# Kernel optimization log

Measured on AMD Instinct MI355X. Metric: run time of the kernel, lower is better.

## Reference

```python
import jax, jax.numpy as jnp
import numpy as np

BN_EPS = 1e-3


def _knn_group(p1, p2, k):
    # p1, p2: [N, 3]. For each point in p1 find k nearest in p2.
    d2 = (jnp.sum(p1 * p1, -1)[:, None] + jnp.sum(p2 * p2, -1)[None, :]
          - 2.0 * (p1 @ p2.T))                      # [N, N]
    _, idx = jax.lax.top_k(-d2, k)                   # [N, k]
    nn = p2[idx]                                     # [N, k, 3]
    resi = nn - p1[:, None, :]                       # [N, k, 3]
    dist = jnp.linalg.norm(resi, axis=-1, keepdims=True)
    feat = jnp.concatenate([resi, dist], axis=-1)    # [N, k, 4]
    return feat, nn


def _conv_bn_relu(x, W, b, g, be):
    # x: [B, Cin, N, K]; 1x1 conv == channel matmul, BN uses batch stats (train mode)
    y = jnp.einsum('oi,binK->bonK', W, x) + b[None, :, None, None]
    m = jnp.mean(y, axis=(0, 2, 3), keepdims=True)
    v = jnp.var(y, axis=(0, 2, 3), keepdims=True)
    y = g[None, :, None, None] * (y - m) * jax.lax.rsqrt(v + BN_EPS) + be[None, :, None, None]
    return jax.nn.relu(y)


def setup_inputs() -> dict:
    key = jax.random.key(0)
    ks = jax.random.split(key, 8)
    B, N, k = 4, 4096, 32
    C = [4, 64, 64, 128]
    inp = {
        'points1': jax.random.normal(ks[0], (B, 3, N), jnp.float32),
        'points2': jax.random.normal(ks[1], (B, 3, N), jnp.float32),
        'k': k,
        't': jax.random.uniform(ks[2], (B,), jnp.float32),
    }
    for i in range(3):
        kw = jax.random.fold_in(ks[3], i)
        inp[f'W{i+1}'] = jax.random.normal(kw, (C[i + 1], C[i]), jnp.float32) * (1.0 / np.sqrt(C[i]))
        inp[f'b{i+1}'] = jnp.zeros((C[i + 1],), jnp.float32)
        inp[f'g{i+1}'] = jnp.ones((C[i + 1],), jnp.float32)
        inp[f'be{i+1}'] = jnp.zeros((C[i + 1],), jnp.float32)
    return inp


def reference(points1, points2, k, t, W1, b1, g1, be1, W2, b2, g2, be2, W3, b3, g3, be3):
    p1 = jnp.transpose(points1, (0, 2, 1))           # [B, N, 3]
    p2 = jnp.transpose(points2, (0, 2, 1))
    knn = jax.vmap(_knn_group, in_axes=(0, 0, None))
    f1, nn1 = knn(p1, p1, k)                          # [B, N, k, 4], [B, N, k, 3]
    f2, nn2 = knn(p1, p2, k)
    feats = jnp.concatenate([f1, f2], axis=2)         # [B, N, 2k, 4]
    grouped = jnp.concatenate([nn1, nn2], axis=2)     # [B, N, 2k, 3]
    x = jnp.transpose(feats, (0, 3, 1, 2))            # [B, 4, N, 2k]
    x = _conv_bn_relu(x, W1, b1, g1, be1)
    x = _conv_bn_relu(x, W2, b2, g2, be2)
    x = _conv_bn_relu(x, W3, b3, g3, be3)             # [B, 128, N, 2k]
    scores = jnp.max(x, axis=1)                       # [B, N, 2k]
    w = jax.nn.softmax(scores, axis=-1)               # [B, N, 2k]
    fused = jnp.einsum('bnk,bnkc->bcn', w, grouped)   # [B, 3, N]
    return fused
```

## Files before the change

### kernel.cpp

```cpp
#include <hip/hip_runtime.h>
#include <hip/hip_bf16.h>

#define B_   4
#define N_   4096
#define KNN_ 32
#define KK_  64
#define MTOT 1048576
#define BN_EPS 1e-3f

typedef unsigned int u32;
typedef unsigned long long u64;
typedef __attribute__((ext_vector_type(8))) short bf16x8;
typedef __attribute__((ext_vector_type(4))) float f32x4;

__device__ __forceinline__ ushort f2bf_bits(float f) {
    u32 b = __float_as_uint(f);
    b += 0x7fffu + ((b >> 16) & 1u);
    return (ushort)(b >> 16);
}

__global__ __launch_bounds__(256, 3) void knn_kernel(
    const float* __restrict__ p1, const float* __restrict__ p2,
    float* __restrict__ feats, float* __restrict__ mom)
{
    __shared__ float2 cxy[N_];
    __shared__ float  cz[N_];
    __shared__ float  part[4][14];

    const int tid  = threadIdx.x;
    const int wave = tid >> 6, lane = tid & 63;
    const int pb    = blockIdx.x / 96;
    const int chunk = blockIdx.x % 96;
    const int pr = pb >> 2, b = pb & 3;
    const int start = (chunk * 4096) / 96;
    const int end   = ((chunk + 1) * 4096) / 96;

    const float* srcb = (pr ? p2 : p1) + (size_t)b * 3 * N_;
    for (int n = tid; n < N_; n += 256) {
        float x = srcb[n], y = srcb[N_ + n], z = srcb[2*N_ + n];
        cxy[n] = make_float2(x, y);
        cz[n]  = z;
    }
    __syncthreads();

    const float* p1b = p1 + (size_t)b * 3 * N_;
    const u64 below = (1ull << lane) - 1ull;

    float mm[14];
    #pragma unroll
    for (int s = 0; s < 14; ++s) mm[s] = 0.f;

    for (int n = start + wave; n < end; n += 4) {
        float qx, qy, qz;
        if (pr == 0) { float2 q = cxy[n]; qx = q.x; qy = q.y; qz = cz[n]; }
        else         { qx = p1b[n]; qy = p1b[N_ + n]; qz = p1b[2*N_ + n]; }
        const float s1 = fmaf(qx, qx, fmaf(qy, qy, qz*qz));

        u32 keys[64];
        u32 a0 = 0xFFFFFFFFu, a1 = 0xFFFFFFFFu, a2 = 0xFFFFFFFFu, a3 = 0xFFFFFFFFu;
        u32 b0 = 0xFFFFFFFFu, b1 = 0xFFFFFFFFu, b2 = 0xFFFFFFFFu, b3 = 0xFFFFFFFFu;
        #pragma unroll
        for (int j = 0; j < 32; ++j) {
            {
                float2 cA = cxy[j * 64 + lane];
                float  zA = cz[j * 64 + lane];
                float cw  = fmaf(cA.x, cA.x, fmaf(cA.y, cA.y, zA*zA));
                float dot = fmaf(qx, cA.x, fmaf(qy, cA.y, qz * zA));
                float d2  = fmaf(-2.0f, dot, s1 + cw);
                u32 u = __float_as_uint(d2);
                u32 key = u ^ (u32)(((int)u >> 31) | 0x80000000);
                keys[j] = key;
                a3 = min(a3, key);
                u32 t;
                t = min(a2, a3); a3 = max(a2, a3); a2 = t;
                t = min(a1, a2); a2 = max(a1, a2); a1 = t;
                t = min(a0, a1); a1 = max(a0, a1); a0 = t;
            }
            {
                float2 cB = cxy[(j + 32) * 64 + lane];
                float  zB = cz[(j + 32) * 64 + lane];
                float cw  = fmaf(cB.x, cB.x, fmaf(cB.y, cB.y, zB*zB));
                float dot = fmaf(qx, cB.x, fmaf(qy, cB.y, qz * zB));
                float d2  = fmaf(-2.0f, dot, s1 + cw);
                u32 u = __float_as_uint(d2);
                u32 key = u ^ (u32)(((int)u >> 31) | 0x80000000);
                keys[j + 32] = key;
                b3 = min(b3, key);
                u32 t;
                t = min(b2, b3); b3 = max(b2, b3); b2 = t;
                t = min(b1, b2); b2 = max(b1, b2); b1 = t;
                t = min(b0, b1); b1 = max(b0, b1); b0 = t;
            }
        }
        u32 k0 = a0, k1 = a1, k2 = a2, k3 = a3;
        #pragma unroll
        for (int m = 0; m < 4; ++m) {
            u32 x = (m == 0) ? b0 : (m == 1) ? b1 : (m == 2) ? b2 : b3;
            k3 = min(k3, x);
            u32 t;
            t = min(k2, k3); k3 = max(k2, k3); k2 = t;
            t = min(k1, k2); k2 = max(k1, k2); k1 = t;
            t = min(k0, k1); k1 = max(k0, k1); k0 = t;
        }

        u32 mn = k0, mx = k3;
        #pragma unroll
        for (int off = 1; off < 64; off <<= 1) {
            mn = min(mn, (u32)__shfl_xor((int)mn, off, 64));
            mx = max(mx, (u32)__shfl_xor((int)mx, off, 64));
        }
        u32 lo = mn, hi = mx;
        while (lo < hi) {
            u32 mid = lo + ((hi - lo) >> 1);
            int c = __popcll(__ballot(k0 <= mid)) + __popcll(__ballot(k1 <= mid))
                  + __popcll(__ballot(k2 <= mid)) + __popcll(__ballot(k3 <= mid));
            if (c >= 32) hi = mid; else lo = mid + 1;
        }
        u32 T = lo;

        int nl;
        if (__ballot(k3 <= T) == 0ull) {
            nl = __popcll(__ballot(k0 < T)) + __popcll(__ballot(k1 < T))
               + __popcll(__ballot(k2 < T)) + __popcll(__ballot(k3 < T));
        } else {
            nl = 0;
            #pragma unroll
            for (int j = 0; j < 64; ++j) nl += __popcll(__ballot(keys[j] < T));
            if (nl > 31) {
                lo = 0u; hi = T;
                while (lo < hi) {
                    u32 mid = lo + ((hi - lo) >> 1);
                    int c = 0;
                    #pragma unroll
                    for (int j = 0; j < 64; ++j) c += __popcll(__ballot(keys[j] <= mid));
                    if (c >= 32) hi = mid; else lo = mid + 1;
                }
                T = lo;
                nl = 0;
                #pragma unroll
                for (int j = 0; j < 64; ++j) nl += __popcll(__ballot(keys[j] < T));
            }
        }
        const int need_eq = 32 - nl;

        float* fout = feats + ((size_t)(b * N_ + n) * KK_ + pr * KNN_) * 4;
        int base = 0, eq_seen = 0;
        #pragma unroll
        for (int j = 0; j < 64; ++j) {
            u32 key = keys[j];
            bool lt = key < T;
            bool eq = key == T;
            u64 mlt = __ballot(lt);
            u64 meq = __ballot(eq);
            if (mlt | meq) {
                int slot = -1;
                if (lt) slot = base + __popcll(mlt & below);
                else if (eq) {
                    int es = eq_seen + __popcll(meq & below);
                    if (es < need_eq) slot = nl + es;
                }
                if (slot >= 0) {
                    float2 cx2 = cxy[j * 64 + lane];
                    float  cz1 = cz[j * 64 + lane];
                    float rx = cx2.x - qx, ry = cx2.y - qy, rz = cz1 - qz;
                    float dist = sqrtf(fmaf(rx, rx, fmaf(ry, ry, rz*rz)));
                    *(float4*)(fout + slot * 4) = make_float4(rx, ry, rz, dist);
                    mm[0] += rx; mm[1] += ry; mm[2] += rz; mm[3] += dist;
                    mm[4]  = fmaf(rx, rx, mm[4]);   mm[5]  = fmaf(rx, ry, mm[5]);
                    mm[6]  = fmaf(rx, rz, mm[6]);   mm[7]  = fmaf(rx, dist, mm[7]);
                    mm[8]  = fmaf(ry, ry, mm[8]);   mm[9]  = fmaf(ry, rz, mm[9]);
                    mm[10] = fmaf(ry, dist, mm[10]); mm[11] = fmaf(rz, rz, mm[11]);
                    mm[12] = fmaf(rz, dist, mm[12]); mm[13] = fmaf(dist, dist, mm[13]);
                }
                base    += __popcll(mlt);
                eq_seen += __popcll(meq);
            }
        }
    }

    #pragma unroll
    for (int s = 0; s < 14; ++s) {
        #pragma unroll
        for (int off = 1; off < 64; off <<= 1) mm[s] += __shfl_xor(mm[s], off, 64);
    }
    if (lane == 0) {
        #pragma unroll
        for (int s = 0; s < 14; ++s) part[wave][s] = mm[s];
    }
    __syncthreads();
    if (tid < 14) {
        float v = part[0][tid] + part[1][tid] + part[2][tid] + part[3][tid];
        atomicAdd(&mom[tid * 16], v);
    }
}

__global__ __launch_bounds__(256) void conv2_mfma(
    const float* __restrict__ feats,
    const float* __restrict__ W1,
    const float* __restrict__ g1, const float* __restrict__ be1,
    const float* __restrict__ W2,
    const float* __restrict__ mom,
    ushort* __restrict__ y2F, float* __restrict__ s2S, float* __restrict__ s2Q)
{
    __shared__ float statS[64], statQ[64];
    const int tid = threadIdx.x;
    const int wid = tid >> 6, l = tid & 63, q = l >> 4, i = l & 15;
    if (tid < 64) { statS[tid] = 0.f; statQ[tid] = 0.f; }

    const float invM = 1.0f / MTOT;
    const float M0 = mom[0*16], M1 = mom[1*16], M2 = mom[2*16], M3 = mom[3*16];
    const float Sxx = mom[4*16],  Sxy = mom[5*16],  Sxz = mom[6*16],  Sxd = mom[7*16];
    const float Syy = mom[8*16],  Syz = mom[9*16],  Syd = mom[10*16];
    const float Szz = mom[11*16], Szd = mom[12*16], Sdd = mom[13*16];

    float4 w1f[16];
    float  c1v[16];
    #pragma unroll
    for (int h = 0; h < 2; ++h)
      #pragma unroll
      for (int j = 0; j < 8; ++j) {
        int ci = h*32 + q*8 + j;
        float w0 = W1[ci*4+0], w1 = W1[ci*4+1], w2 = W1[ci*4+2], w3 = W1[ci*4+3];
        float meanf = (w0*M0 + w1*M1 + w2*M2 + w3*M3) * invM;
        float qq = w0*(w0*Sxx + 2.f*(w1*Sxy + w2*Sxz + w3*Sxd))
                 + w1*(w1*Syy + 2.f*(w2*Syz + w3*Syd))
                 + w2*(w2*Szz + 2.f*w3*Szd)
                 + w3*w3*Sdd;
        float var = qq * invM - meanf * meanf;
        float sc  = g1[ci] * rsqrtf(var + BN_EPS);
        w1f[h*8+j] = make_float4(sc*w0, sc*w1, sc*w2, sc*w3);
        c1v[h*8+j] = fmaf(-sc, meanf, be1[ci]);
      }
    bf16x8 a2[4][2];
    #pragma unroll
    for (int t = 0; t < 4; ++t)
      #pragma unroll
      for (int h = 0; h < 2; ++h)
        #pragma unroll
        for (int j = 0; j < 8; ++j)
          a2[t][h][j] = (short)f2bf_bits(W2[(t*16 + i)*64 + h*32 + q*8 + j]);

    float ssum[16], ssq[16];
    #pragma unroll
    for (int s = 0; s < 16; ++s) { ssum[s] = 0.f; ssq[s] = 0.f; }
    __syncthreads();

    for (int r16 = 0; r16 < 16; ++r16) {
        const int row = blockIdx.x * 16 + r16;
        float4 f = ((const float4*)feats)[row*64 + wid*16 + i];
        bf16x8 xb[2];
        #pragma unroll
        for (int h = 0; h < 2; ++h)
          #pragma unroll
          for (int j = 0; j < 8; ++j) {
            float4 w = w1f[h*8+j];
            float x = fmaxf(fmaf(w.x, f.x, fmaf(w.y, f.y, fmaf(w.z, f.z, fmaf(w.w, f.w, c1v[h*8+j])))), 0.f);
            xb[h][j] = (short)f2bf_bits(x);
          }
        f32x4 acc[4];
        #pragma unroll
        for (int t = 0; t < 4; ++t) acc[t] = (f32x4){0.f,0.f,0.f,0.f};
        #pragma unroll
        for (int t = 0; t < 4; ++t) {
            acc[t] = __builtin_amdgcn_mfma_f32_16x16x32_bf16(a2[t][0], xb[0], acc[t], 0, 0, 0);
            acc[t] = __builtin_amdgcn_mfma_f32_16x16x32_bf16(a2[t][1], xb[1], acc[t], 0, 0, 0);
        }
        ushort* wp = y2F + row*4096 + wid*1024 + q*64 + i*4;
        #pragma unroll
        for (int t = 0; t < 4; ++t) {
            #pragma unroll
            for (int reg = 0; reg < 4; ++reg) {
                float y = acc[t][reg];
                ssum[t*4+reg] += y;
                ssq[t*4+reg]  = fmaf(y, y, ssq[t*4+reg]);
            }
            uint2 pk;
            pk.x = (u32)f2bf_bits(acc[t][0]) | ((u32)f2bf_bits(acc[t][1]) << 16);
            pk.y = (u32)f2bf_bits(acc[t][2]) | ((u32)f2bf_bits(acc[t][3]) << 16);
            *(uint2*)(wp + t*256) = pk;
        }
    }
    #pragma unroll
    for (int s = 0; s < 16; ++s) {
        #pragma unroll
        for (int off = 1; off < 16; off <<= 1) {
            ssum[s] += __shfl_xor(ssum[s], off, 64);
            ssq[s]  += __shfl_xor(ssq[s],  off, 64);
        }
    }
    if (i == 0) {
        #pragma unroll
        for (int s = 0; s < 16; ++s) {
            int co = (s >> 2)*16 + q*4 + (s & 3);
            atomicAdd(&statS[co], ssum[s]);
            atomicAdd(&statQ[co], ssq[s]);
        }
    }
    __syncthreads();
    if (tid < 64) { atomicAdd(&s2S[tid], statS[tid]); atomicAdd(&s2Q[tid], statQ[tid]); }
}

template<bool FINAL>
__global__ __launch_bounds__(256) void conv3_mfma(
    const ushort* __restrict__ y2F,
    const float* __restrict__ g2, const float* __restrict__ be2,
    const float* __restrict__ W3,
    const float* __restrict__ g3, const float* __restrict__ be3,
    const float* __restrict__ s2S, const float* __restrict__ s2Q,
    float* __restrict__ s3S, float* __restrict__ s3Q,
    const float4* __restrict__ feats4, const float* __restrict__ p1,
    float* __restrict__ outp)
{
    __shared__ float statS[128], statQ[128];
    __shared__ float sc3L[128], sh3L[128];
    __shared__ float scoreL[2][64];

    const int tid = threadIdx.x;
    const int wid = tid >> 6, l = tid & 63, q = l >> 4, i = l & 15;

    if (!FINAL) {
        if (tid < 128) { statS[tid] = 0.f; statQ[tid] = 0.f; }
    } else if (tid < 128) {
        float m  = s3S[tid] * (1.0f / MTOT);
        float v  = s3Q[tid] * (1.0f / MTOT) - m * m;
        float sc = g3[tid] * rsqrtf(v + BN_EPS);
        sc3L[tid] = sc;
        sh3L[tid] = fmaf(-sc, m, be3[tid]);
    }

    float sc2v[16], sh2v[16];
    #pragma unroll
    for (int h = 0; h < 2; ++h)
      #pragma unroll
      for (int j = 0; j < 8; ++j) {
        int ci = h*32 + q*8 + j;
        float m  = s2S[ci] * (1.0f / MTOT);
        float v  = s2Q[ci] * (1.0f / MTOT) - m * m;
        float sc = g2[ci] * rsqrtf(v + BN_EPS);
        sc2v[h*8+j] = sc;
        sh2v[h*8+j] = fmaf(-sc, m, be2[ci]);
      }
    bf16x8 a3[8][2];
    #pragma unroll
    for (int t = 0; t < 8; ++t)
      #pragma unroll
      for (int h = 0; h < 2; ++h)
        #pragma unroll
        for (int j = 0; j < 8; ++j)
          a3[t][h][j] = (short)f2bf_bits(W3[(t*16 + i)*64 + h*32 + q*8 + j]);

    float ssum[32], ssq[32];
    if (!FINAL) {
        #pragma unroll
        for (int s = 0; s < 32; ++s) { ssum[s] = 0.f; ssq[s] = 0.f; }
    }
    __syncthreads();

    for (int r16 = 0; r16 < 16; ++r16) {
        const int row = blockIdx.x * 16 + r16;
        const ushort* rp = y2F + row*4096 + wid*1024 + q*128 + i*4;
        uint2 u00 = *(const uint2*)(rp);
        uint2 u01 = *(const uint2*)(rp + 64);
        uint2 u10 = *(const uint2*)(rp + 512);
        uint2 u11 = *(const uint2*)(rp + 576);

        bf16x8 xb[2];
        #pragma unroll
        for (int h = 0; h < 2; ++h) {
            u32 w0 = (h == 0) ? u00.x : u10.x;
            u32 w1 = (h == 0) ? u00.y : u10.y;
            u32 w2 = (h == 0) ? u01.x : u11.x;
            u32 w3 = (h == 0) ? u01.y : u11.y;
            float xf[8];
            xf[0] = __uint_as_float(w0 << 16); xf[1] = __uint_as_float(w0 & 0xffff0000u);
            xf[2] = __uint_as_float(w1 << 16); xf[3] = __uint_as_float(w1 & 0xffff0000u);
            xf[4] = __uint_as_float(w2 << 16); xf[5] = __uint_as_float(w2 & 0xffff0000u);
            xf[6] = __uint_as_float(w3 << 16); xf[7] = __uint_as_float(w3 & 0xffff0000u);
            #pragma unroll
            for (int j = 0; j < 8; ++j) {
                float x = fmaxf(fmaf(sc2v[h*8+j], xf[j], sh2v[h*8+j]), 0.f);
                xb[h][j] = (short)f2bf_bits(x);
            }
        }
        f32x4 acc[8];
        #pragma unroll
        for (int t = 0; t < 8; ++t) acc[t] = (f32x4){0.f,0.f,0.f,0.f};
        #pragma unroll
        for (int t = 0; t < 8; ++t) {
            acc[t] = __builtin_amdgcn_mfma_f32_16x16x32_bf16(a3[t][0], xb[0], acc[t], 0, 0, 0);
            acc[t] = __builtin_amdgcn_mfma_f32_16x16x32_bf16(a3[t][1], xb[1], acc[t], 0, 0, 0);
        }

        if (!FINAL) {
            #pragma unroll
            for (int t = 0; t < 8; ++t)
              #pragma unroll
              for (int reg = 0; reg < 4; ++reg) {
                float y = acc[t][reg];
                ssum[t*4+reg] += y;
                ssq[t*4+reg]  = fmaf(y, y, ssq[t*4+reg]);
              }
        } else {
            float mx = -3.4e38f;
            #pragma unroll
            for (int t = 0; t < 8; ++t) {
                float4 s4 = *(const float4*)&sc3L[t*16 + q*4];
                float4 h4 = *(const float4*)&sh3L[t*16 + q*4];
                mx = fmaxf(mx, fmaf(s4.x, acc[t][0], h4.x));
                mx = fmaxf(mx, fmaf(s4.y, acc[t][1], h4.y));
                mx = fmaxf(mx, fmaf(s4.z, acc[t][2], h4.z));
                mx = fmaxf(mx, fmaf(s4.w, acc[t][3], h4.w));
            }
            mx = fmaxf(mx, __shfl_xor(mx, 16, 64));
            mx = fmaxf(mx, __shfl_xor(mx, 32, 64));
            mx = fmaxf(mx, 0.f);
            if (q == 0) scoreL[r16 & 1][wid*16 + i] = mx;
            __syncthreads();
            if (wid == 0) {
                float sc = scoreL[r16 & 1][l];
                float m2 = sc;
                #pragma unroll
                for (int off = 1; off < 64; off <<= 1) m2 = fmaxf(m2, __shfl_xor(m2, off, 64));
                float e = __expf(sc - m2);
                float se = e;
                #pragma unroll
                for (int off = 1; off < 64; off <<= 1) se += __shfl_xor(se, off, 64);
                float w = e / se;
                const int bb = row >> 12, n = row & 4095;
                float qx = p1[(size_t)bb*3*N_ + n];
                float qy = p1[(size_t)bb*3*N_ + N_ + n];
                float qz = p1[(size_t)bb*3*N_ + 2*N_ + n];
                float4 f4 = feats4[row*64 + l];
                float ox = w * (f4.x + qx), oy = w * (f4.y + qy), oz = w * (f4.z + qz);
                #pragma unroll
                for (int off = 1; off < 64; off <<= 1) {
                    ox += __shfl_xor(ox, off, 64);
                    oy += __shfl_xor(oy, off, 64);
                    oz += __shfl_xor(oz, off, 64);
                }
                if (l == 0) {
                    outp[bb*3*N_ + 0*N_ + n] = ox;
                    outp[bb*3*N_ + 1*N_ + n] = oy;
                    outp[bb*3*N_ + 2*N_ + n] = oz;
                }
            }
        }
    }

    if (!FINAL) {
        #pragma unroll
        for (int s = 0; s < 32; ++s) {
            #pragma unroll
            for (int off = 1; off < 16; off <<= 1) {
                ssum[s] += __shfl_xor(ssum[s], off, 64);
                ssq[s]  += __shfl_xor(ssq[s],  off, 64);
            }
        }
        if (i == 0) {
            #pragma unroll
            for (int s = 0; s < 32; ++s) {
                int co = (s >> 2)*16 + q*4 + (s & 3);
                atomicAdd(&statS[co], ssum[s]);
                atomicAdd(&statQ[co], ssq[s]);
            }
        }
        __syncthreads();
        if (tid < 128) { atomicAdd(&s3S[tid], statS[tid]); atomicAdd(&s3Q[tid], statQ[tid]); }
    }
}

extern "C" void kernel_launch(void* const* d_in, const int* in_sizes, int n_in,
                              void* d_out, int out_size, void* d_ws, size_t ws_size,
                              hipStream_t stream)
{
    const float* p1  = (const float*)d_in[0];
    const float* p2  = (const float*)d_in[1];
    const float* W1  = (const float*)d_in[4];
    const float* g1  = (const float*)d_in[6];
    const float* be1 = (const float*)d_in[7];
    const float* W2  = (const float*)d_in[8];
    const float* g2  = (const float*)d_in[10];
    const float* be2 = (const float*)d_in[11];
    const float* W3  = (const float*)d_in[12];
    const float* g3  = (const float*)d_in[14];
    const float* be3 = (const float*)d_in[15];

    char* ws = (char*)d_ws;
    const size_t OFF_FEATS = 4096;
    const size_t OFF_Y2    = OFF_FEATS + (size_t)MTOT * 4 * 4;
    const size_t NEEDED    = OFF_Y2 + (size_t)MTOT * 64 * 2;
    if (ws_size < NEEDED) return;

    float* s2S = (float*)(ws + 512);  float* s2Q = (float*)(ws + 768);
    float* s3S = (float*)(ws + 1024); float* s3Q = (float*)(ws + 1536);
    float* mom = (float*)(ws + 2048);
    float* feats = (float*)(ws + OFF_FEATS);
    ushort* y2F  = (ushort*)(ws + OFF_Y2);

    hipMemsetAsync(ws, 0, 4096, stream);

    knn_kernel<<<768, 256, 0, stream>>>(p1, p2, feats, mom);
    conv2_mfma<<<1024, 256, 0, stream>>>(feats, W1, g1, be1, W2, mom,
                                         y2F, s2S, s2Q);
    conv3_mfma<false><<<1024, 256, 0, stream>>>(y2F, g2, be2, W3, g3, be3,
                                                s2S, s2Q, s3S, s3Q,
                                                nullptr, nullptr, nullptr);
    conv3_mfma<true><<<1024, 256, 0, stream>>>(y2F, g2, be2, W3, g3, be3,
                                               s2S, s2Q, s3S, s3Q,
                                               (const float4*)feats, p1,
                                               (float*)d_out);
}
```

Baseline: 511.8 us.

## Write BN2-ReLU activations back in place and split conv3 output channels across waves

The conv3 stats pass now applies the BN2 scale/shift, ReLU and bf16 rounding, then writes the activated values back into the y2 buffer in place. The final pass can then feed those values straight into the MFMAs without redoing the normalization. Work is also repartitioned so each wave handles two point-tiles and half of the 128 output channels, which halves the A-fragment register footprint (a3 drops from 8x2 to 4x2). The cost is an extra 128 MB of bf16 global writes in the stats pass. There is also an in-place read-then-write hazard, guarded only by a block-level __syncthreads, that depends on the two wave halves reading identical addresses.

Result: faster. 477.4 us (-6.7%).

```diff
diff --git a/kernel.cpp b/kernel.cpp
--- a/kernel.cpp
+++ b/kernel.cpp
@@ -300,33 +300,18 @@
     if (tid < 64) { atomicAdd(&s2S[tid], statS[tid]); atomicAdd(&s2Q[tid], statQ[tid]); }
 }
 
-template<bool FINAL>
-__global__ __launch_bounds__(256) void conv3_mfma(
-    const ushort* __restrict__ y2F,
+__global__ __launch_bounds__(256) void conv3_stats(
+    ushort* __restrict__ y2F,
     const float* __restrict__ g2, const float* __restrict__ be2,
     const float* __restrict__ W3,
-    const float* __restrict__ g3, const float* __restrict__ be3,
     const float* __restrict__ s2S, const float* __restrict__ s2Q,
-    float* __restrict__ s3S, float* __restrict__ s3Q,
-    const float4* __restrict__ feats4, const float* __restrict__ p1,
-    float* __restrict__ outp)
+    float* __restrict__ s3S, float* __restrict__ s3Q)
 {
     __shared__ float statS[128], statQ[128];
-    __shared__ float sc3L[128], sh3L[128];
-    __shared__ float scoreL[2][64];
-
     const int tid = threadIdx.x;
-    const int wid = tid >> 6, l = tid & 63, q = l >> 4, i = l & 15;
-
-    if (!FINAL) {
-        if (tid < 128) { statS[tid] = 0.f; statQ[tid] = 0.f; }
-    } else if (tid < 128) {
-        float m  = s3S[tid] * (1.0f / MTOT);
-        float v  = s3Q[tid] * (1.0f / MTOT) - m * m;
-        float sc = g3[tid] * rsqrtf(v + BN_EPS);
-        sc3L[tid] = sc;
-        sh3L[tid] = fmaf(-sc, m, be3[tid]);
-    }
+    const int w = tid >> 6, l = tid & 63, q = l >> 4, i = l & 15;
+    const int ph = w >> 1, oh = w & 1;
+    if (tid < 128) { statS[tid] = 0.f; statQ[tid] = 0.f; }
 
     float sc2v[16], sh2v[16];
     #pragma unroll
@@ -340,132 +325,188 @@
         sc2v[h*8+j] = sc;
         sh2v[h*8+j] = fmaf(-sc, m, be2[ci]);
       }
-    bf16x8 a3[8][2];
-    #pragma unroll
-    for (int t = 0; t < 8; ++t)
+    bf16x8 a3[4][2];
+    #pragma unroll
+    for (int t = 0; t < 4; ++t)
       #pragma unroll
       for (int h = 0; h < 2; ++h)
         #pragma unroll
         for (int j = 0; j < 8; ++j)
-          a3[t][h][j] = (short)f2bf_bits(W3[(t*16 + i)*64 + h*32 + q*8 + j]);
-
-    float ssum[32], ssq[32];
-    if (!FINAL) {
-        #pragma unroll
-        for (int s = 0; s < 32; ++s) { ssum[s] = 0.f; ssq[s] = 0.f; }
-    }
-    __syncthreads();
+          a3[t][h][j] = (short)f2bf_bits(W3[((oh*4 + t)*16 + i)*64 + h*32 + q*8 + j]);
+
+    float ssum[16], ssq[16];
+    #pragma unroll
+    for (int s = 0; s < 16; ++s) { ssum[s] = 0.f; ssq[s] = 0.f; }
 
     for (int r16 = 0; r16 < 16; ++r16) {
         const int row = blockIdx.x * 16 + r16;
-        const ushort* rp = y2F + row*4096 + wid*1024 + q*128 + i*4;
-        uint2 u00 = *(const uint2*)(rp);
-        uint2 u01 = *(const uint2*)(rp + 64);
-        uint2 u10 = *(const uint2*)(rp + 512);
-        uint2 u11 = *(const uint2*)(rp + 576);
-
-        bf16x8 xb[2];
-        #pragma unroll
-        for (int h = 0; h < 2; ++h) {
-            u32 w0 = (h == 0) ? u00.x : u10.x;
-            u32 w1 = (h == 0) ? u00.y : u10.y;
-            u32 w2 = (h == 0) ? u01.x : u11.x;
-            u32 w3 = (h == 0) ? u01.y : u11.y;
-            float xf[8];
-            xf[0] = __uint_as_float(w0 << 16); xf[1] = __uint_as_float(w0 & 0xffff0000u);
-            xf[2] = __uint_as_float(w1 << 16); xf[3] = __uint_as_float(w1 & 0xffff0000u);
-            xf[4] = __uint_as_float(w2 << 16); xf[5] = __uint_as_float(w2 & 0xffff0000u);
-            xf[6] = __uint_as_float(w3 << 16); xf[7] = __uint_as_float(w3 & 0xffff0000u);
-            #pragma unroll
-            for (int j = 0; j < 8; ++j) {
-                float x = fmaxf(fmaf(sc2v[h*8+j], xf[j], sh2v[h*8+j]), 0.f);
-                xb[h][j] = (short)f2bf_bits(x);
-            }
-        }
-        f32x4 acc[8];
-        #pragma unroll
-        for (int t = 0; t < 8; ++t) acc[t] = (f32x4){0.f,0.f,0.f,0.f};
-        #pragma unroll
-        for (int t = 0; t < 8; ++t) {
-            acc[t] = __builtin_amdgcn_mfma_f32_16x16x32_bf16(a3[t][0], xb[0], acc[t], 0, 0, 0);
-            acc[t] = __builtin_amdgcn_mfma_f32_16x16x32_bf16(a3[t][1], xb[1], acc[t], 0, 0, 0);
-        }
-
-        if (!FINAL) {
-            #pragma unroll
-            for (int t = 0; t < 8; ++t)
-              #pragma unroll
-              for (int reg = 0; reg < 4; ++reg) {
-                float y = acc[t][reg];
-                ssum[t*4+reg] += y;
-                ssq[t*4+reg]  = fmaf(y, y, ssq[t*4+reg]);
-              }
-        } else {
+        ushort* rp0 = y2F + row*4096 + (2*ph)*1024 + q*128 + i*4;
+        ushort* rp1 = rp0 + 1024;
+        uint2 a00 = *(const uint2*)(rp0);       uint2 a01 = *(const uint2*)(rp0 + 64);
+        uint2 a10 = *(const uint2*)(rp0 + 512); uint2 a11 = *(const uint2*)(rp0 + 576);
+        uint2 b00 = *(const uint2*)(rp1);       uint2 b01 = *(const uint2*)(rp1 + 64);
+        uint2 b10 = *(const uint2*)(rp1 + 512); uint2 b11 = *(const uint2*)(rp1 + 576);
+
+        bf16x8 xa[2], xc[2];
+        #pragma unroll
+        for (int pt2 = 0; pt2 < 2; ++pt2) {
+            uint2 v00 = pt2 ? b00 : a00, v01 = pt2 ? b01 : a01;
+            uint2 v10 = pt2 ? b10 : a10, v11 = pt2 ? b11 : a11;
+            bf16x8* dst = pt2 ? xc : xa;
+            #pragma unroll
+            for (int h = 0; h < 2; ++h) {
+                u32 w0 = h ? v10.x : v00.x, w1 = h ? v10.y : v00.y;
+                u32 w2 = h ? v11.x : v01.x, w3 = h ? v11.y : v01.y;
+                float xf[8];
+                xf[0] = __uint_as_float(w0 << 16); xf[1] = __uint_as_float(w0 & 0xffff0000u);
+                xf[2] = __uint_as_float(w1 << 16); xf[3] = __uint_as_float(w1 & 0xffff0000u);
+                xf[4] = __uint_as_float(w2 << 16); xf[5] = __uint_as_float(w2 & 0xffff0000u);
+                xf[6] = __uint_as_float(w3 << 16); xf[7] = __uint_as_float(w3 & 0xffff0000u);
+                #pragma unroll
+                for (int j = 0; j < 8; ++j) {
+                    float x = fmaxf(fmaf(sc2v[h*8+j], xf[j], sh2v[h*8+j]), 0.f);
+                    dst[h][j] = (short)f2bf_bits(x);
+                }
+            }
+        }
+        __syncthreads();
+        if (oh == 0) {
+            uint4 ua0 = *(uint4*)&xa[0], ua1 = *(uint4*)&xa[1];
+            uint4 uc0 = *(uint4*)&xc[0], uc1 = *(uint4*)&xc[1];
+            *(uint2*)(rp0)       = make_uint2(ua0.x, ua0.y);
+            *(uint2*)(rp0 + 64)  = make_uint2(ua0.z, ua0.w);
+            *(uint2*)(rp0 + 512) = make_uint2(ua1.x, ua1.y);
+            *(uint2*)(rp0 + 576) = make_uint2(ua1.z, ua1.w);
+            *(uint2*)(rp1)       = make_uint2(uc0.x, uc0.y);
+            *(uint2*)(rp1 + 64)  = make_uint2(uc0.z, uc0.w);
+            *(uint2*)(rp1 + 512) = make_uint2(uc1.x, uc1.y);
+            *(uint2*)(rp1 + 576) = make_uint2(uc1.z, uc1.w);
+        }
+        #pragma unroll
+        for (int t = 0; t < 4; ++t) {
+            f32x4 A = (f32x4){0.f,0.f,0.f,0.f};
+            A = __builtin_amdgcn_mfma_f32_16x16x32_bf16(a3[t][0], xa[0], A, 0, 0, 0);
+            A = __builtin_amdgcn_mfma_f32_16x16x32_bf16(a3[t][1], xa[1], A, 0, 0, 0);
+            f32x4 Bv = (f32x4){0.f,0.f,0.f,0.f};
+            Bv = __builtin_amdgcn_mfma_f32_16x16x32_bf16(a3[t][0], xc[0], Bv, 0, 0, 0);
+            Bv = __builtin_amdgcn_mfma_f32_16x16x32_bf16(a3[t][1], xc[1], Bv, 0, 0, 0);
+            #pragma unroll
+            for (int reg = 0; reg < 4; ++reg) {
+                float ya = A[reg], yb = Bv[reg];
+                ssum[t*4+reg] += ya + yb;
+                ssq[t*4+reg]  = fmaf(ya, ya, fmaf(yb, yb, ssq[t*4+reg]));
+            }
+        }
+    }
+    #pragma unroll
+    for (int s = 0; s < 16; ++s) {
+        #pragma unroll
+        for (int off = 1; off < 16; off <<= 1) {
+            ssum[s] += __shfl_xor(ssum[s], off, 64);
+            ssq[s]  += __shfl_xor(ssq[s],  off, 64);
+        }
+    }
+    if (i == 0) {
+        #pragma unroll
+        for (int s = 0; s < 16; ++s) {
+            int co = oh*64 + (s >> 2)*16 + q*4 + (s & 3);
+            atomicAdd(&statS[co], ssum[s]);
+            atomicAdd(&statQ[co], ssq[s]);
+        }
+    }
+    __syncthreads();
+    if (tid < 128) { atomicAdd(&s3S[tid], statS[tid]); atomicAdd(&s3Q[tid], statQ[tid]); }
+}
+
+__global__ __launch_bounds__(256) void conv3_final(
+    const ushort* __restrict__ x3F,
+    const float* __restrict__ W3,
+    const float* __restrict__ g3, const float* __restrict__ be3,
+    const float* __restrict__ s3S, const float* __restrict__ s3Q,
+    const float4* __restrict__ feats4, const float* __restrict__ p1,
+    float* __restrict__ outp)
+{
+    __shared__ float sc3L[128], sh3L[128];
+    __shared__ float s2L[2][2][64];
+    const int tid = threadIdx.x;
+    const int w = tid >> 6, l = tid & 63, q = l >> 4, i = l & 15;
+    const int ph = w >> 1, oh = w & 1;
+
+    if (tid < 128) {
+        float m  = s3S[tid] * (1.0f / MTOT);
+        float v  = s3Q[tid] * (1.0f / MTOT) - m * m;
+        float sc = g3[tid] * rsqrtf(v + BN_EPS);
+        sc3L[tid] = sc;
+        sh3L[tid] = fmaf(-sc, m, be3[tid]);
+    }
+    bf16x8 a3[4][2];
+    #pragma unroll
+    for (int t = 0; t < 4; ++t)
+      #pragma unroll
+      for (int h = 0; h < 2; ++h)
+        #pragma unroll
+        for (int j = 0; j < 8; ++j)
+          a3[t][h][j] = (short)f2bf_bits(W3[((oh*4 + t)*16 + i)*64 + h*32 + q*8 + j]);
+    __syncthreads();
+
+    for (int r16 = 0; r16 < 16; ++r16) {
+        const int row = blockIdx.x * 16 + r16;
+        #pragma unroll
+        for (int pt2 = 0; pt2 < 2; ++pt2) {
+            const int pt = 2*ph + pt2;
+            const ushort* rp = x3F + row*4096 + pt*1024 + q*128 + i*4;
+            uint2 u00 = *(const uint2*)(rp);       uint2 u01 = *(const uint2*)(rp + 64);
+            uint2 u10 = *(const uint2*)(rp + 512); uint2 u11 = *(const uint2*)(rp + 576);
+            uint4 v0 = make_uint4(u00.x, u00.y, u01.x, u01.y);
+            uint4 v1 = make_uint4(u10.x, u10.y, u11.x, u11.y);
+            bf16x8 xb0 = *(bf16x8*)&v0, xb1 = *(bf16x8*)&v1;
             float mx = -3.4e38f;
             #pragma unroll
-            for (int t = 0; t < 8; ++t) {
-                float4 s4 = *(const float4*)&sc3L[t*16 + q*4];
-                float4 h4 = *(const float4*)&sh3L[t*16 + q*4];
-                mx = fmaxf(mx, fmaf(s4.x, acc[t][0], h4.x));
-                mx = fmaxf(mx, fmaf(s4.y, acc[t][1], h4.y));
-                mx = fmaxf(mx, fmaf(s4.z, acc[t][2], h4.z));
-                mx = fmaxf(mx, fmaf(s4.w, acc[t][3], h4.w));
+            for (int t = 0; t < 4; ++t) {
+                f32x4 a = (f32x4){0.f,0.f,0.f,0.f};
+                a = __builtin_amdgcn_mfma_f32_16x16x32_bf16(a3[t][0], xb0, a, 0, 0, 0);
+                a = __builtin_amdgcn_mfma_f32_16x16x32_bf16(a3[t][1], xb1, a, 0, 0, 0);
+                const int co = oh*64 + t*16 + q*4;
+                float4 s4 = *(const float4*)&sc3L[co];
+                float4 h4 = *(const float4*)&sh3L[co];
+                mx = fmaxf(mx, fmaf(s4.x, a[0], h4.x));
+                mx = fmaxf(mx, fmaf(s4.y, a[1], h4.y));
+                mx = fmaxf(mx, fmaf(s4.z, a[2], h4.z));
+                mx = fmaxf(mx, fmaf(s4.w, a[3], h4.w));
             }
             mx = fmaxf(mx, __shfl_xor(mx, 16, 64));
             mx = fmaxf(mx, __shfl_xor(mx, 32, 64));
-            mx = fmaxf(mx, 0.f);
-            if (q == 0) scoreL[r16 & 1][wid*16 + i] = mx;
-            __syncthreads();
-            if (wid == 0) {
-                float sc = scoreL[r16 & 1][l];
-                float m2 = sc;
-                #pragma unroll
-                for (int off = 1; off < 64; off <<= 1) m2 = fmaxf(m2, __shfl_xor(m2, off, 64));
-                float e = __expf(sc - m2);
-                float se = e;
-                #pragma unroll
-                for (int off = 1; off < 64; off <<= 1) se += __shfl_xor(se, off, 64);
-                float w = e / se;
-                const int bb = row >> 12, n = row & 4095;
-                float qx = p1[(size_t)bb*3*N_ + n];
-                float qy = p1[(size_t)bb*3*N_ + N_ + n];
-                float qz = p1[(size_t)bb*3*N_ + 2*N_ + n];
-                float4 f4 = feats4[row*64 + l];
-                float ox = w * (f4.x + qx), oy = w * (f4.y + qy), oz = w * (f4.z + qz);
-                #pragma unroll
-                for (int off = 1; off < 64; off <<= 1) {
-                    ox += __shfl_xor(ox, off, 64);
-                    oy += __shfl_xor(oy, off, 64);
-                    oz += __shfl_xor(oz, off, 64);
-                }
-                if (l == 0) {
-                    outp[bb*3*N_ + 0*N_ + n] = ox;
-                    outp[bb*3*N_ + 1*N_ + n] = oy;
-                    outp[bb*3*N_ + 2*N_ + n] = oz;
-                }
-            }
-        }
-    }
-
-    if (!FINAL) {
-        #pragma unroll
-        for (int s = 0; s < 32; ++s) {
-            #pragma unroll
-            for (int off = 1; off < 16; off <<= 1) {
-                ssum[s] += __shfl_xor(ssum[s], off, 64);
-                ssq[s]  += __shfl_xor(ssq[s],  off, 64);
-            }
-        }
-        if (i == 0) {
-            #pragma unroll
-            for (int s = 0; s < 32; ++s) {
-                int co = (s >> 2)*16 + q*4 + (s & 3);
-                atomicAdd(&statS[co], ssum[s]);
-                atomicAdd(&statQ[co], ssq[s]);
-            }
+            if (q == 0) s2L[r16 & 1][oh][pt*16 + i] = mx;
         }
         __syncthreads();
-        if (tid < 128) { atomicAdd(&s3S[tid], statS[tid]); atomicAdd(&s3Q[tid], statQ[tid]); }
+        if (w == 0) {
+            float sc = fmaxf(fmaxf(s2L[r16 & 1][0][l], s2L[r16 & 1][1][l]), 0.f);
+            float m2 = sc;
+            #pragma unroll
+            for (int off = 1; off < 64; off <<= 1) m2 = fmaxf(m2, __shfl_xor(m2, off, 64));
+            float e = __expf(sc - m2);
+            float se = e;
+            #pragma unroll
+            for (int off = 1; off < 64; off <<= 1) se += __shfl_xor(se, off, 64);
+            float wgt = e / se;
+            const int bb = row >> 12, n = row & 4095;
+            float qx = p1[(size_t)bb*3*N_ + n];
+            float qy = p1[(size_t)bb*3*N_ + N_ + n];
+            float qz = p1[(size_t)bb*3*N_ + 2*N_ + n];
+            float4 f4 = feats4[row*64 + l];
+            float ox = wgt * (f4.x + qx), oy = wgt * (f4.y + qy), oz = wgt * (f4.z + qz);
+            #pragma unroll
+            for (int off = 1; off < 64; off <<= 1) {
+                ox += __shfl_xor(ox, off, 64);
+                oy += __shfl_xor(oy, off, 64);
+                oz += __shfl_xor(oz, off, 64);
+            }
+            if (l == 0) {
+                outp[bb*3*N_ + 0*N_ + n] = ox;
+                outp[bb*3*N_ + 1*N_ + n] = oy;
+                outp[bb*3*N_ + 2*N_ + n] = oz;
+            }
+        }
     }
 }
 
@@ -502,11 +543,9 @@
     knn_kernel<<<768, 256, 0, stream>>>(p1, p2, feats, mom);
     conv2_mfma<<<1024, 256, 0, stream>>>(feats, W1, g1, be1, W2, mom,
                                          y2F, s2S, s2Q);
-    conv3_mfma<false><<<1024, 256, 0, stream>>>(y2F, g2, be2, W3, g3, be3,
-                                                s2S, s2Q, s3S, s3Q,
-                                                nullptr, nullptr, nullptr);
-    conv3_mfma<true><<<1024, 256, 0, stream>>>(y2F, g2, be2, W3, g3, be3,
-                                               s2S, s2Q, s3S, s3Q,
-                                               (const float4*)feats, p1,
-                                               (float*)d_out);
+    conv3_stats<<<1024, 256, 0, stream>>>(y2F, g2, be2, W3,
+                                          s2S, s2Q, s3S, s3Q);
+    conv3_final<<<1024, 256, 0, stream>>>(y2F, W3, g3, be3, s3S, s3Q,
+                                          (const float4*)feats, p1,
+                                          (float*)d_out);
 }
```
